# Performance work log

Measured on AMD Instinct MI355X. Metric: run time of the kernel, lower is better.

## Reference

```python
import jax, jax.numpy as jnp
import numpy as np

HEADS = 16
D_MODEL = 1024
D_K = D_MODEL // HEADS


def setup_inputs() -> dict:
    key = jax.random.key(0)
    ks = jax.random.split(key, 8)
    B, S = 4, 2048
    scale = 1.0 / np.sqrt(D_MODEL)
    return {
        "queries": jax.random.normal(ks[0], (B, S, D_MODEL), dtype=jnp.float32),
        "keys": jax.random.normal(ks[1], (B, S, D_MODEL), dtype=jnp.float32),
        "values": jax.random.normal(ks[2], (B, S, D_MODEL), dtype=jnp.float32),
        # Per-head projection weights, stacked over heads: [H, d_model, d_k]
        "Wq": jax.random.normal(ks[3], (HEADS, D_MODEL, D_K), dtype=jnp.float32) * scale,
        "Wk": jax.random.normal(ks[4], (HEADS, D_MODEL, D_K), dtype=jnp.float32) * scale,
        "Wv": jax.random.normal(ks[5], (HEADS, D_MODEL, D_K), dtype=jnp.float32) * scale,
        "Wout": jax.random.normal(ks[6], (D_MODEL, D_MODEL), dtype=jnp.float32) * scale,
        "bout": jax.random.normal(ks[7], (D_MODEL,), dtype=jnp.float32) * 0.01,
    }


def reference(queries, keys, values, Wq, Wk, Wv, Wout, bout):
    # Per-head linear projections (torch Linear: x @ W.T, here W stored as [H, d_model, d_k])
    q = jnp.einsum("bsd,hdk->bhsk", queries, Wq)   # [B,H,S,d_k]
    k = jnp.einsum("btd,hdk->bhtk", keys, Wk)      # [B,H,T,d_k]
    v = jnp.einsum("btd,hdv->bhtv", values, Wv)    # [B,H,T,d_v]
    scores = jnp.einsum("bhsk,bhtk->bhst", q, k) / jnp.sqrt(jnp.float32(D_K))
    probs = jax.nn.softmax(scores, axis=-1)        # [B,H,S,T]
    wv = jnp.einsum("bhst,bhtv->bhsv", probs, v)   # [B,H,S,d_v]
    # concat heads along last dim: [B,S,H*d_v] == [B,S,d_model]
    B, H, S, Dv = wv.shape
    concat = jnp.transpose(wv, (0, 2, 1, 3)).reshape(B, S, H * Dv)
    return concat @ Wout.T + bout
```

## Files before the change

kernel.cpp:

```cpp
#include <hip/hip_runtime.h>
#include <hip/hip_bf16.h>
#include <stdint.h>

#define DM 1024
#define SZ ((size_t)8192*1024)
#define WSZ ((size_t)1024*1024)

typedef float  f32x4  __attribute__((ext_vector_type(4)));
typedef float  f32x16 __attribute__((ext_vector_type(16)));
typedef __bf16 bf16x8 __attribute__((ext_vector_type(8)));
typedef __bf16 bf16x2 __attribute__((ext_vector_type(2)));
typedef short  s16x8  __attribute__((ext_vector_type(8)));
typedef unsigned int u32;
typedef unsigned int u32x4 __attribute__((ext_vector_type(4)));

typedef const __attribute__((address_space(1))) void* gas_ptr;
typedef __attribute__((address_space(3))) void* las_ptr;

static __device__ __forceinline__ f32x4 mfma16(s16x8 a, s16x8 b, f32x4 c){
  return __builtin_amdgcn_mfma_f32_16x16x32_bf16(
      __builtin_bit_cast(bf16x8, a), __builtin_bit_cast(bf16x8, b), c, 0, 0, 0);
}
static __device__ __forceinline__ f32x16 mfma32(s16x8 a, s16x8 b, f32x16 c){
  return __builtin_amdgcn_mfma_f32_32x32x16_bf16(
      __builtin_bit_cast(bf16x8, a), __builtin_bit_cast(bf16x8, b), c, 0, 0, 0);
}

static __device__ __forceinline__ u32 pack2(float a, float b){
  bf16x2 v = { (__bf16)a, (__bf16)b };
  return __builtin_bit_cast(u32, v);
}
static __device__ __forceinline__ short f2bf(float f){
  __bf16 v = (__bf16)f;
  return __builtin_bit_cast(short, v);
}

static __device__ __forceinline__ void gload_lds16(void* l, const void* g){
  __builtin_amdgcn_global_load_lds((gas_ptr)g, (las_ptr)l, 16, 0, 0);
}

#define QSCALE 0.1803368801111444f


__global__ void convert_misc(const float* __restrict__ q, const float* __restrict__ k,
                             const float* __restrict__ v, const float* __restrict__ wo,
                             short* __restrict__ ws){
  const size_t n8_in  = (3*SZ)/8;
  const size_t n8_tot = n8_in + WSZ/8;
  size_t stride = (size_t)gridDim.x * blockDim.x;
  for (size_t c = (size_t)blockIdx.x*blockDim.x + threadIdx.x; c < n8_tot; c += stride){
    const float* src; short* dst;
    if (c < n8_in){
      size_t e = c*8;
      int s = (int)(e / SZ);
      size_t off = e - (size_t)s*SZ;
      src = (s==0 ? q : (s==1 ? k : v)) + off;
      dst = ws + e;
    } else {
      size_t off = (c - n8_in)*8;
      src = wo + off;
      dst = ws + 6*SZ + 3*WSZ + off;
    }
    float4 a = *(const float4*)src;
    float4 b = *(const float4*)(src + 4);
    uint4 o;
    o.x = pack2(a.x, a.y); o.y = pack2(a.z, a.w);
    o.z = pack2(b.x, b.y); o.w = pack2(b.z, b.w);
    *(uint4*)dst = o;
  }
}

__global__ void convert_wqkv(const float* __restrict__ wq, const float* __restrict__ wk,
                             const float* __restrict__ wv, short* __restrict__ ws){
  __shared__ float tile[64][65];
  int bid = blockIdx.x;
  int sel = bid >> 8;
  int h   = (bid >> 4) & 15;
  int dt  = bid & 15;
  const float* W = sel==0 ? wq : (sel==1 ? wk : wv);
  float sc = sel==0 ? QSCALE : 1.0f;
  short* Bt = ws + 6*SZ + (size_t)sel*WSZ;
  int tid = threadIdx.x;
  int r = tid >> 4, c4 = (tid & 15)*4;
  int d0 = dt*64;
  #pragma unroll
  for (int i=0;i<4;i++){
    int d = r + i*16;
    float4 vv = *(const float4*)&W[(size_t)h*65536 + (size_t)(d0+d)*64 + c4];
    tile[d][c4+0]=vv.x*sc; tile[d][c4+1]=vv.y*sc; tile[d][c4+2]=vv.z*sc; tile[d][c4+3]=vv.w*sc;
  }
  __syncthreads();
  #pragma unroll
  for (int i=0;i<4;i++){
    int kk = r + i*16;
    unsigned int lo = pack2(tile[c4+0][kk], tile[c4+1][kk]);
    unsigned int hi = pack2(tile[c4+2][kk], tile[c4+3][kk]);
    *(uint2*)&Bt[(size_t)(h*64+kk)*1024 + d0 + c4] = make_uint2(lo, hi);
  }
}


static __device__ __forceinline__ void gemm_core(
    const short* __restrict__ A, const short* __restrict__ Bt,
    int bm, int bn, short* As, short* Bs, f32x4 acc[4][4])
{
  int tid = threadIdx.x;
  int w = tid>>6, lane = tid&63;
  int wm = w>>1, wn = w&1;
  int col = lane&15, kg = lane>>4;
  int rs = w*16 + (lane>>2);
  int ch = lane&3;

  auto stage = [&](int buf, int kt){
    #pragma unroll
    for (int it=0; it<2; ++it){
      int r = rs + it*64;
      gload_lds16(As + buf*4096 + r*32 + ch*8,
                  A + (size_t)(bm*128 + r)*1024 + kt*32 + ch*8);
    }
    #pragma unroll
    for (int it=0; it<2; ++it){
      int r = rs + it*64;
      gload_lds16(Bs + buf*4096 + r*32 + ch*8,
                  Bt + (size_t)(bn*128 + r)*1024 + kt*32 + ch*8);
    }
  };

  const f32x4 fzero = {0.f,0.f,0.f,0.f};
  #pragma unroll
  for (int mf=0; mf<4; ++mf)
    #pragma unroll
    for (int nf=0; nf<4; ++nf)
      acc[mf][nf] = fzero;

  stage(0, 0);
  int buf = 0;
  for (int kt=0; kt<32; ++kt){
    __syncthreads();
    if (kt < 31) stage(buf^1, kt+1);
    s16x8 af[4], bfr[4];
    #pragma unroll
    for (int mf=0; mf<4; ++mf)
      af[mf] = *(const s16x8*)(As + buf*4096 + (wm*64 + mf*16 + col)*32 + kg*8);
    #pragma unroll
    for (int nf=0; nf<4; ++nf)
      bfr[nf] = *(const s16x8*)(Bs + buf*4096 + (wn*64 + nf*16 + col)*32 + kg*8);
    #pragma unroll
    for (int mf=0; mf<4; ++mf)
      #pragma unroll
      for (int nf=0; nf<4; ++nf)
        acc[mf][nf] = mfma16(af[mf], bfr[nf], acc[mf][nf]);
    buf ^= 1;
  }
}

__global__ __launch_bounds__(256,2) void gemm_qkv(short* __restrict__ ws){
  __shared__ __align__(16) short As[2*4096];
  __shared__ __align__(16) short Bs[2*4096];
  int bid = blockIdx.x;
  bid = (bid & 7)*192 + (bid >> 3);
  int bm = bid / 24, bnq = bid % 24;
  int sel = bnq >> 3, bn = bnq & 7;
  const short* A  = ws + (size_t)sel*SZ;
  const short* Bt = ws + 6*SZ + (size_t)sel*WSZ;
  f32x4 acc[4][4];
  gemm_core(A, Bt, bm, bn, As, Bs, acc);

  int tid = threadIdx.x, w = tid>>6, lane = tid&63;
  int wm=w>>1, wn=w&1, col=lane&15, kg=lane>>4;
  if (sel == 0){
    short* O = ws + 3*SZ;
    #pragma unroll
    for (int mf=0; mf<4; ++mf){
      int gr0 = bm*128 + wm*64 + mf*16 + kg*4;
      #pragma unroll
      for (int nf=0; nf<4; ++nf){
        int gc = bn*128 + wn*64 + nf*16 + col;
        #pragma unroll
        for (int r=0; r<4; ++r)
          O[(size_t)(gr0+r)*1024 + gc] = f2bf(acc[mf][nf][r]);
      }
    }
  } else if (sel == 1){
    short* Kt = ws + 4*SZ;
    #pragma unroll
    for (int mf=0; mf<4; ++mf){
      int gr0 = bm*128 + wm*64 + mf*16 + kg*4;
      int b = gr0 >> 11, s0 = gr0 & 2047;
      int ts = s0 >> 5, t0 = s0 & 31;
      #pragma unroll
      for (int nf=0; nf<4; ++nf){
        int gc = bn*128 + wn*64 + nf*16 + col;
        int h = gc >> 6, d = gc & 63;
        size_t base = ((size_t)((b*16+h)*64 + ts))*2048 + (size_t)((d>>3)*32)*8 + (d&7);
        #pragma unroll
        for (int r=0; r<4; ++r)
          Kt[base + (size_t)(t0+r)*8] = f2bf(acc[mf][nf][r]);
      }
    }
  } else {
    short* Vt = ws + 5*SZ;
    #pragma unroll
    for (int mf=0; mf<4; ++mf){
      int gr0 = bm*128 + wm*64 + mf*16 + kg*4;
      int b = gr0 >> 11, s0 = gr0 & 2047;
      int ts = s0 >> 5, c2 = (s0 >> 3) & 3, j0 = s0 & 7;
      #pragma unroll
      for (int nf=0; nf<4; ++nf){
        int gc = bn*128 + wn*64 + nf*16 + col;
        int h = gc >> 6, dv = gc & 63;
        unsigned int lo = pack2(acc[mf][nf][0], acc[mf][nf][1]);
        unsigned int hi = pack2(acc[mf][nf][2], acc[mf][nf][3]);
        size_t addr = ((size_t)((b*16+h)*64 + ts))*2048 + (size_t)(c2*64 + dv)*8 + j0;
        *(uint2*)&Vt[addr] = make_uint2(lo, hi);
      }
    }
  }
}

__global__ __launch_bounds__(256,2) void gemm_out(const short* __restrict__ cc,
                                                  const short* __restrict__ BtO,
                                                  const float* __restrict__ bias,
                                                  float* __restrict__ out){
  __shared__ __align__(16) short As[2*4096];
  __shared__ __align__(16) short Bs[2*4096];
  int bid = blockIdx.x;
  bid = (bid & 7)*64 + (bid >> 3);
  int bm = bid >> 3, bn = bid & 7;
  f32x4 acc[4][4];
  gemm_core(cc, BtO, bm, bn, As, Bs, acc);

  int tid = threadIdx.x, w=tid>>6, lane=tid&63;
  int wm=w>>1, wn=w&1, col=lane&15, kg=lane>>4;
  #pragma unroll
  for (int nf=0; nf<4; ++nf){
    int gc = bn*128 + wn*64 + nf*16 + col;
    float bb = bias[gc];
    #pragma unroll
    for (int mf=0; mf<4; ++mf){
      int gr0 = bm*128 + wm*64 + mf*16 + kg*4;
      #pragma unroll
      for (int r=0; r<4; ++r)
        out[(size_t)(gr0+r)*1024 + gc] = acc[mf][nf][r] + bb;
    }
  }
}

__global__ __launch_bounds__(256,2) void attn(const short* __restrict__ qp,
                                              const short* __restrict__ kpT,
                                              const short* __restrict__ vTt,
                                              short* __restrict__ cc){
  __shared__ __align__(16) short Ks[2][2048];
  __shared__ __align__(16) short Vs[2][2048];
  int bid = blockIdx.x;
  bid = (bid & 7)*64 + (bid >> 3);
  int qb = bid & 7, h = (bid>>3) & 15, b = bid >> 7;
  int tid = threadIdx.x, w = tid>>6, lane = tid&63;
  int ql = lane & 31, hi = lane >> 5;
  int qbase = qb*256 + w*64;

  const short* qg = qp + ((size_t)(b*2048 + qbase + ql))*1024 + h*64;
  s16x8 qf[2][4];
  #pragma unroll
  for (int qt=0; qt<2; ++qt)
    #pragma unroll
    for (int ks=0; ks<4; ++ks)
      qf[qt][ks] = *(const s16x8*)(qg + qt*32*1024 + ks*16 + hi*8);

  const short* ktb = kpT + ((size_t)((b*16 + h)*64))*2048;
  const short* vtb = vTt + ((size_t)((b*16 + h)*64))*2048;

  int koff = hi*512 + ql*16;
  int voff = hi*1024 + ql*16;

  const short* sgb = (w < 2) ? ktb : vtb;
  short* ldb = (w < 2) ? &Ks[0][0] : &Vs[0][0];
  int jj = (w & 1) * 1024;
  auto stage = [&](int buf, int ti){
    const short* src = sgb + (size_t)ti*2048 + jj + lane*8;
    short* dst = ldb + buf*2048 + jj + lane*8;
    gload_lds16(dst, src);
    gload_lds16(dst + 512, src + 512);
  };

  const f32x16 z16 = {0.f,0.f,0.f,0.f,0.f,0.f,0.f,0.f,
                      0.f,0.f,0.f,0.f,0.f,0.f,0.f,0.f};
  f32x16 o[2][2] = {{z16, z16}, {z16, z16}};
  float l0 = 0.f, l1 = 0.f;

  auto packP = [&](f32x16& s, s16x8* pb){
    u32 a0 = pack2(s[0], s[1]),  b0 = pack2(s[2], s[3]);
    u32 c0 = pack2(s[4], s[5]),  d0 = pack2(s[6], s[7]);
    asm("v_permlane32_swap_b32 %0, %1" : "+v"(a0), "+v"(c0));
    asm("v_permlane32_swap_b32 %0, %1" : "+v"(b0), "+v"(d0));
    u32x4 t0v = {a0, b0, c0, d0};
    pb[0] = __builtin_bit_cast(s16x8, t0v);
    u32 a1 = pack2(s[8], s[9]),   b1 = pack2(s[10], s[11]);
    u32 c1 = pack2(s[12], s[13]), d1 = pack2(s[14], s[15]);
    asm("v_permlane32_swap_b32 %0, %1" : "+v"(a1), "+v"(c1));
    asm("v_permlane32_swap_b32 %0, %1" : "+v"(b1), "+v"(d1));
    u32x4 t1v = {a1, b1, c1, d1};
    pb[1] = __builtin_bit_cast(s16x8, t1v);
  };

  auto body = [&](int buf){
    const char* kt = (const char*)Ks + buf*4096;
    const char* vt = (const char*)Vs + buf*4096;
    f32x16 s0 = z16, s1 = z16;
    __builtin_amdgcn_s_setprio(1);
    #pragma unroll
    for (int ks=0; ks<4; ++ks){
      s16x8 kf = *(const s16x8*)(kt + koff + ks*1024);
      s0 = mfma32(kf, qf[0][ks], s0);
      s1 = mfma32(kf, qf[1][ks], s1);
    }
    __builtin_amdgcn_s_setprio(0);

    float la=0.f, lb=0.f, lc=0.f, ld=0.f;
    #pragma unroll
    for (int i=0;i<16;i+=4){
      s0[i]   = __builtin_amdgcn_exp2f(s0[i]);   la += s0[i];
      s0[i+1] = __builtin_amdgcn_exp2f(s0[i+1]); lb += s0[i+1];
      s0[i+2] = __builtin_amdgcn_exp2f(s0[i+2]); lc += s0[i+2];
      s0[i+3] = __builtin_amdgcn_exp2f(s0[i+3]); ld += s0[i+3];
    }
    l0 += (la+lb)+(lc+ld);
    float le=0.f, lf=0.f, lg=0.f, lh=0.f;
    #pragma unroll
    for (int i=0;i<16;i+=4){
      s1[i]   = __builtin_amdgcn_exp2f(s1[i]);   le += s1[i];
      s1[i+1] = __builtin_amdgcn_exp2f(s1[i+1]); lf += s1[i+1];
      s1[i+2] = __builtin_amdgcn_exp2f(s1[i+2]); lg += s1[i+2];
      s1[i+3] = __builtin_amdgcn_exp2f(s1[i+3]); lh += s1[i+3];
    }
    l1 += (le+lf)+(lg+lh);

    s16x8 pb0[2], pb1[2];
    packP(s0, pb0);
    packP(s1, pb1);

    __builtin_amdgcn_s_setprio(1);
    #pragma unroll
    for (int ks2=0; ks2<2; ++ks2){
      #pragma unroll
      for (int dvt=0; dvt<2; ++dvt){
        s16x8 vf = *(const s16x8*)(vt + voff + ks2*2048 + dvt*512);
        o[0][dvt] = mfma32(vf, pb0[ks2], o[0][dvt]);
        o[1][dvt] = mfma32(vf, pb1[ks2], o[1][dvt]);
      }
    }
    __builtin_amdgcn_s_setprio(0);
  };

  stage(0, 0);
  for (int ti = 0; ti < 64; ti += 2){
    __syncthreads();
    stage(1, ti+1);
    body(0);
    __syncthreads();
    if (ti+2 < 64) stage(0, ti+2);
    body(1);
  }

  l0 += __shfl_xor(l0, 32);
  l1 += __shfl_xor(l1, 32);
  float rc0 = 1.0f / l0, rc1 = 1.0f / l1;
  #pragma unroll
  for (int qt=0; qt<2; ++qt){
    float rcl = qt ? rc1 : rc0;
    short* og = cc + ((size_t)(b*2048 + qbase + qt*32 + ql))*1024 + h*64;
    #pragma unroll
    for (int dvt=0; dvt<2; ++dvt){
      #pragma unroll
      for (int s=0; s<4; ++s){
        int dv0 = dvt*32 + s*8 + hi*4;
        uint2 wd;
        wd.x = pack2(o[qt][dvt][s*4+0]*rcl, o[qt][dvt][s*4+1]*rcl);
        wd.y = pack2(o[qt][dvt][s*4+2]*rcl, o[qt][dvt][s*4+3]*rcl);
        *(uint2*)&og[dv0] = wd;
      }
    }
  }
}


extern "C" void kernel_launch(void* const* d_in, const int* in_sizes, int n_in,
                              void* d_out, int out_size, void* d_ws, size_t ws_size,
                              hipStream_t stream){
  const float* q  = (const float*)d_in[0];
  const float* k  = (const float*)d_in[1];
  const float* v  = (const float*)d_in[2];
  const float* wq = (const float*)d_in[3];
  const float* wk = (const float*)d_in[4];
  const float* wv = (const float*)d_in[5];
  const float* wo = (const float*)d_in[6];
  const float* bo = (const float*)d_in[7];
  short* ws = (short*)d_ws;
  float* out = (float*)d_out;

  size_t needed = (6*SZ + 4*WSZ)*sizeof(short);
  if (ws_size < needed) return;

  convert_misc<<<2048, 256, 0, stream>>>(q, k, v, wo, ws);
  convert_wqkv<<<768, 256, 0, stream>>>(wq, wk, wv, ws);
  gemm_qkv<<<1536, 256, 0, stream>>>(ws);
  attn<<<512, 256, 0, stream>>>(ws + 3*SZ, ws + 4*SZ, ws + 5*SZ, ws);
  gemm_out<<<512, 256, 0, stream>>>(ws, ws + 6*SZ + 3*WSZ, bo, out);
}
```

Baseline: 201.4 us.

## Fuse fp32-to-bf16 input conversion into QKV GEMM, split attention over keys, swizzle LDS

The QKV projection GEMM now reads fp32 activations directly, converting them to bf16 in registers before writing to LDS. This removes the separate pass that converted the large input tensors. LDS tiles in both GEMM cores use an XOR swizzle on 16-byte chunks to reduce bank conflicts on the fragment reads. Attention is split into two key halves per query block, doubling the grid and raising the occupancy hint, and a new merge kernel combines the fp32 partial outputs and row sums. The split adds extra global traffic for the partials plus one more kernel launch. It relies on the max-free softmax so the two halves can simply be added.

```diff
diff --git a/kernel.cpp b/kernel.cpp
--- a/kernel.cpp
+++ b/kernel.cpp
@@ -41,33 +41,19 @@
 
 #define QSCALE 0.1803368801111444f
 
-
-__global__ void convert_misc(const float* __restrict__ q, const float* __restrict__ k,
-                             const float* __restrict__ v, const float* __restrict__ wo,
-                             short* __restrict__ ws){
-  const size_t n8_in  = (3*SZ)/8;
-  const size_t n8_tot = n8_in + WSZ/8;
-  size_t stride = (size_t)gridDim.x * blockDim.x;
-  for (size_t c = (size_t)blockIdx.x*blockDim.x + threadIdx.x; c < n8_tot; c += stride){
-    const float* src; short* dst;
-    if (c < n8_in){
-      size_t e = c*8;
-      int s = (int)(e / SZ);
-      size_t off = e - (size_t)s*SZ;
-      src = (s==0 ? q : (s==1 ? k : v)) + off;
-      dst = ws + e;
-    } else {
-      size_t off = (c - n8_in)*8;
-      src = wo + off;
-      dst = ws + 6*SZ + 3*WSZ + off;
-    }
-    float4 a = *(const float4*)src;
-    float4 b = *(const float4*)(src + 4);
-    uint4 o;
-    o.x = pack2(a.x, a.y); o.y = pack2(a.z, a.w);
-    o.z = pack2(b.x, b.y); o.w = pack2(b.z, b.w);
-    *(uint4*)dst = o;
-  }
+#define PO_OFF_SHORTS (6*SZ + 4*WSZ)
+#define PO_SPLIT_FLOATS ((size_t)512*16384)
+#define PL_FLOATS ((size_t)262144)
+
+
+__global__ void convert_wo(const float* __restrict__ wo, short* __restrict__ dst){
+  size_t i = ((size_t)blockIdx.x*blockDim.x + threadIdx.x)*8;
+  float4 a = *(const float4*)(wo + i);
+  float4 b = *(const float4*)(wo + i + 4);
+  uint4 o;
+  o.x = pack2(a.x, a.y); o.y = pack2(a.z, a.w);
+  o.z = pack2(b.x, b.y); o.w = pack2(b.z, b.w);
+  *(uint4*)(dst + i) = o;
 }
 
 __global__ void convert_wqkv(const float* __restrict__ wq, const float* __restrict__ wk,
@@ -100,7 +86,7 @@
 }
 
 
-static __device__ __forceinline__ void gemm_core(
+static __device__ __forceinline__ void gemm_core_bf16(
     const short* __restrict__ A, const short* __restrict__ Bt,
     int bm, int bn, short* As, short* Bs, f32x4 acc[4][4])
 {
@@ -110,19 +96,20 @@
   int col = lane&15, kg = lane>>4;
   int rs = w*16 + (lane>>2);
   int ch = lane&3;
+  int chs = ch ^ (rs & 3);
 
   auto stage = [&](int buf, int kt){
     #pragma unroll
     for (int it=0; it<2; ++it){
       int r = rs + it*64;
       gload_lds16(As + buf*4096 + r*32 + ch*8,
-                  A + (size_t)(bm*128 + r)*1024 + kt*32 + ch*8);
+                  A + (size_t)(bm*128 + r)*1024 + kt*32 + chs*8);
     }
     #pragma unroll
     for (int it=0; it<2; ++it){
       int r = rs + it*64;
       gload_lds16(Bs + buf*4096 + r*32 + ch*8,
-                  Bt + (size_t)(bn*128 + r)*1024 + kt*32 + ch*8);
+                  Bt + (size_t)(bn*128 + r)*1024 + kt*32 + chs*8);
     }
   };
 
@@ -132,6 +119,8 @@
     #pragma unroll
     for (int nf=0; nf<4; ++nf)
       acc[mf][nf] = fzero;
+
+  int fbase = col*32 + ((kg ^ (col&3))<<3);
 
   stage(0, 0);
   int buf = 0;
@@ -141,10 +130,10 @@
     s16x8 af[4], bfr[4];
     #pragma unroll
     for (int mf=0; mf<4; ++mf)
-      af[mf] = *(const s16x8*)(As + buf*4096 + (wm*64 + mf*16 + col)*32 + kg*8);
+      af[mf] = *(const s16x8*)(As + buf*4096 + (wm*64 + mf*16)*32 + fbase);
     #pragma unroll
     for (int nf=0; nf<4; ++nf)
-      bfr[nf] = *(const s16x8*)(Bs + buf*4096 + (wn*64 + nf*16 + col)*32 + kg*8);
+      bfr[nf] = *(const s16x8*)(Bs + buf*4096 + (wn*64 + nf*16)*32 + fbase);
     #pragma unroll
     for (int mf=0; mf<4; ++mf)
       #pragma unroll
@@ -154,17 +143,97 @@
   }
 }
 
-__global__ __launch_bounds__(256,2) void gemm_qkv(short* __restrict__ ws){
+
+static __device__ __forceinline__ void gemm_core_f32A(
+    const float* __restrict__ A, const short* __restrict__ Bt,
+    int bm, int bn, short* As, short* Bs, f32x4 acc[4][4])
+{
+  int tid = threadIdx.x;
+  int w = tid>>6, lane = tid&63;
+  int wm = w>>1, wn = w&1;
+  int col = lane&15, kg = lane>>4;
+
+  int ra = tid>>1;
+  int ca0 = (tid&1)*2;
+  const float* ag = A + (size_t)(bm*128 + ra)*1024 + ca0*8;
+  int ac0 = (ca0   ^ (ra & 3));
+  int ac1 = ((ca0+1) ^ (ra & 3));
+
+  int rs = w*16 + (lane>>2);
+  int ch = lane&3;
+  int chs = ch ^ (rs & 3);
+  const short* bg = Bt + (size_t)(bn*128 + rs)*1024 + chs*8;
+
+  float4 rA0, rA1, rA2, rA3;
+  auto issueA = [&](int kt){
+    const float4* p = (const float4*)(ag + kt*32);
+    rA0 = p[0]; rA1 = p[1]; rA2 = p[2]; rA3 = p[3];
+  };
+  auto writeA = [&](int buf){
+    uint4 v0, v1;
+    v0.x = pack2(rA0.x, rA0.y); v0.y = pack2(rA0.z, rA0.w);
+    v0.z = pack2(rA1.x, rA1.y); v0.w = pack2(rA1.z, rA1.w);
+    v1.x = pack2(rA2.x, rA2.y); v1.y = pack2(rA2.z, rA2.w);
+    v1.z = pack2(rA3.x, rA3.y); v1.w = pack2(rA3.z, rA3.w);
+    *(uint4*)(As + buf*4096 + ra*32 + ac0*8) = v0;
+    *(uint4*)(As + buf*4096 + ra*32 + ac1*8) = v1;
+  };
+  auto stageB = [&](int buf, int kt){
+    gload_lds16(Bs + buf*4096 + rs*32 + ch*8, bg + kt*32);
+    gload_lds16(Bs + buf*4096 + (rs+64)*32 + ch*8, bg + (size_t)64*1024 + kt*32);
+  };
+
+  const f32x4 fzero = {0.f,0.f,0.f,0.f};
+  #pragma unroll
+  for (int mf=0; mf<4; ++mf)
+    #pragma unroll
+    for (int nf=0; nf<4; ++nf)
+      acc[mf][nf] = fzero;
+
+  int fbase = col*32 + ((kg ^ (col&3))<<3);
+
+  issueA(0);
+  stageB(0, 0);
+  writeA(0);
+  issueA(1);
+  int buf = 0;
+  for (int kt=0; kt<32; ++kt){
+    __syncthreads();
+    if (kt < 31){
+      stageB(buf^1, kt+1);
+      writeA(buf^1);
+      if (kt < 30) issueA(kt+2);
+    }
+    s16x8 af[4], bfr[4];
+    #pragma unroll
+    for (int mf=0; mf<4; ++mf)
+      af[mf] = *(const s16x8*)(As + buf*4096 + (wm*64 + mf*16)*32 + fbase);
+    #pragma unroll
+    for (int nf=0; nf<4; ++nf)
+      bfr[nf] = *(const s16x8*)(Bs + buf*4096 + (wn*64 + nf*16)*32 + fbase);
+    #pragma unroll
+    for (int mf=0; mf<4; ++mf)
+      #pragma unroll
+      for (int nf=0; nf<4; ++nf)
+        acc[mf][nf] = mfma16(af[mf], bfr[nf], acc[mf][nf]);
+    buf ^= 1;
+  }
+}
+
+__global__ __launch_bounds__(256,2) void gemm_qkv(const float* __restrict__ q,
+                                                  const float* __restrict__ k,
+                                                  const float* __restrict__ v,
+                                                  short* __restrict__ ws){
   __shared__ __align__(16) short As[2*4096];
   __shared__ __align__(16) short Bs[2*4096];
   int bid = blockIdx.x;
   bid = (bid & 7)*192 + (bid >> 3);
   int bm = bid / 24, bnq = bid % 24;
   int sel = bnq >> 3, bn = bnq & 7;
-  const short* A  = ws + (size_t)sel*SZ;
+  const float* A  = sel==0 ? q : (sel==1 ? k : v);
   const short* Bt = ws + 6*SZ + (size_t)sel*WSZ;
   f32x4 acc[4][4];
-  gemm_core(A, Bt, bm, bn, As, Bs, acc);
+  gemm_core_f32A(A, Bt, bm, bn, As, Bs, acc);
 
   int tid = threadIdx.x, w = tid>>6, lane = tid&63;
   int wm=w>>1, wn=w&1, col=lane&15, kg=lane>>4;
@@ -228,7 +297,7 @@
   bid = (bid & 7)*64 + (bid >> 3);
   int bm = bid >> 3, bn = bid & 7;
   f32x4 acc[4][4];
-  gemm_core(cc, BtO, bm, bn, As, Bs, acc);
+  gemm_core_bf16(cc, BtO, bm, bn, As, Bs, acc);
 
   int tid = threadIdx.x, w=tid>>6, lane=tid&63;
   int wm=w>>1, wn=w&1, col=lane&15, kg=lane>>4;
@@ -246,15 +315,17 @@
   }
 }
 
-__global__ __launch_bounds__(256,2) void attn(const short* __restrict__ qp,
+__global__ __launch_bounds__(256,4) void attn(const short* __restrict__ qp,
                                               const short* __restrict__ kpT,
                                               const short* __restrict__ vTt,
-                                              short* __restrict__ cc){
+                                              float* __restrict__ pO,
+                                              float* __restrict__ pl){
   __shared__ __align__(16) short Ks[2][2048];
   __shared__ __align__(16) short Vs[2][2048];
   int bid = blockIdx.x;
-  bid = (bid & 7)*64 + (bid >> 3);
-  int qb = bid & 7, h = (bid>>3) & 15, b = bid >> 7;
+  bid = (bid & 7)*128 + (bid >> 3);
+  int ts = bid & 1, qb = (bid >> 1) & 7, bh = bid >> 4;
+  int h = bh & 15, b = bh >> 4;
   int tid = threadIdx.x, w = tid>>6, lane = tid&63;
   int ql = lane & 31, hi = lane >> 5;
   int qbase = qb*256 + w*64;
@@ -267,8 +338,8 @@
     for (int ks=0; ks<4; ++ks)
       qf[qt][ks] = *(const s16x8*)(qg + qt*32*1024 + ks*16 + hi*8);
 
-  const short* ktb = kpT + ((size_t)((b*16 + h)*64))*2048;
-  const short* vtb = vTt + ((size_t)((b*16 + h)*64))*2048;
+  const short* ktb = kpT + ((size_t)(bh*64))*2048;
+  const short* vtb = vTt + ((size_t)(bh*64))*2048;
 
   int koff = hi*512 + ql*16;
   int voff = hi*1024 + ql*16;
@@ -352,32 +423,70 @@
     __builtin_amdgcn_s_setprio(0);
   };
 
-  stage(0, 0);
-  for (int ti = 0; ti < 64; ti += 2){
+  int tb = ts*32;
+  stage(0, tb);
+  for (int ti = 0; ti < 32; ti += 2){
     __syncthreads();
-    stage(1, ti+1);
+    stage(1, tb+ti+1);
     body(0);
     __syncthreads();
-    if (ti+2 < 64) stage(0, ti+2);
+    if (ti+2 < 32) stage(0, tb+ti+2);
     body(1);
   }
 
   l0 += __shfl_xor(l0, 32);
   l1 += __shfl_xor(l1, 32);
-  float rc0 = 1.0f / l0, rc1 = 1.0f / l1;
+  if (hi == 0){
+    float* pls = pl + (size_t)ts*131072 + bh*2048 + qb*256 + w*64 + ql;
+    pls[0]  = l0;
+    pls[32] = l1;
+  }
+  float* po = pO + (size_t)ts*PO_SPLIT_FLOATS + (size_t)(bh*8+qb)*16384 + tid*4;
+  #pragma unroll
+  for (int qt=0; qt<2; ++qt)
+    #pragma unroll
+    for (int dvt=0; dvt<2; ++dvt)
+      #pragma unroll
+      for (int i4=0; i4<4; ++i4){
+        int g = qt*8 + dvt*4 + i4;
+        float4 vv;
+        vv.x = o[qt][dvt][i4*4+0]; vv.y = o[qt][dvt][i4*4+1];
+        vv.z = o[qt][dvt][i4*4+2]; vv.w = o[qt][dvt][i4*4+3];
+        *(float4*)(po + (size_t)g*1024) = vv;
+      }
+}
+
+__global__ __launch_bounds__(256) void attn_merge(const float* __restrict__ pO,
+                                                  const float* __restrict__ pl,
+                                                  short* __restrict__ cc){
+  int bid = blockIdx.x;
+  int bh = bid >> 3, qb = bid & 7;
+  int b = bh >> 4, h = bh & 15;
+  int tid = threadIdx.x, w = tid>>6, lane = tid&63;
+  int ql = lane & 31, hi = lane >> 5;
+  int qbase = qb*256 + w*64;
+  const float* p0 = pO + (size_t)bid*16384 + tid*4;
+  const float* p1 = p0 + PO_SPLIT_FLOATS;
+  float rcl[2];
   #pragma unroll
   for (int qt=0; qt<2; ++qt){
-    float rcl = qt ? rc1 : rc0;
+    int li = bh*2048 + qb*256 + w*64 + qt*32 + ql;
+    rcl[qt] = 1.0f / (pl[li] + pl[131072 + li]);
+  }
+  #pragma unroll
+  for (int qt=0; qt<2; ++qt){
     short* og = cc + ((size_t)(b*2048 + qbase + qt*32 + ql))*1024 + h*64;
     #pragma unroll
     for (int dvt=0; dvt<2; ++dvt){
       #pragma unroll
-      for (int s=0; s<4; ++s){
-        int dv0 = dvt*32 + s*8 + hi*4;
+      for (int i4=0; i4<4; ++i4){
+        int g = qt*8 + dvt*4 + i4;
+        float4 a = *(const float4*)(p0 + (size_t)g*1024);
+        float4 c = *(const float4*)(p1 + (size_t)g*1024);
         uint2 wd;
-        wd.x = pack2(o[qt][dvt][s*4+0]*rcl, o[qt][dvt][s*4+1]*rcl);
-        wd.y = pack2(o[qt][dvt][s*4+2]*rcl, o[qt][dvt][s*4+3]*rcl);
-        *(uint2*)&og[dv0] = wd;
+        wd.x = pack2((a.x+c.x)*rcl[qt], (a.y+c.y)*rcl[qt]);
+        wd.y = pack2((a.z+c.z)*rcl[qt], (a.w+c.w)*rcl[qt]);
+        *(uint2*)&og[dvt*32 + i4*8 + hi*4] = wd;
       }
     }
   }
@@ -398,12 +507,16 @@
   short* ws = (short*)d_ws;
   float* out = (float*)d_out;
 
-  size_t needed = (6*SZ + 4*WSZ)*sizeof(short);
+  float* pO = (float*)(ws + PO_OFF_SHORTS);
+  float* pl = pO + 2*PO_SPLIT_FLOATS;
+  size_t needed = PO_OFF_SHORTS*sizeof(short)
+                + (2*PO_SPLIT_FLOATS + 2*PL_FLOATS)*sizeof(float);
   if (ws_size < needed) return;
 
-  convert_misc<<<2048, 256, 0, stream>>>(q, k, v, wo, ws);
+  convert_wo<<<512, 256, 0, stream>>>(wo, ws + 6*SZ + 3*WSZ);
   convert_wqkv<<<768, 256, 0, stream>>>(wq, wk, wv, ws);
-  gemm_qkv<<<1536, 256, 0, stream>>>(ws);
-  attn<<<512, 256, 0, stream>>>(ws + 3*SZ, ws + 4*SZ, ws + 5*SZ, ws);
+  gemm_qkv<<<1536, 256, 0, stream>>>(q, k, v, ws);
+  attn<<<1024, 256, 0, stream>>>(ws + 3*SZ, ws + 4*SZ, ws + 5*SZ, pO, pl);
+  attn_merge<<<512, 256, 0, stream>>>(pO, pl, ws);
   gemm_out<<<512, 256, 0, stream>>>(ws, ws + 6*SZ + 3*WSZ, bo, out);
 }
```

After: 347.4 us. 1.72x slower.
